# Kernel optimization log

Hardware: AMD Instinct MI355X
Metric: run time of the kernel (lower is better)

## Reference

```python
import jax, jax.numpy as jnp
import numpy as np

NUM_HEADS = 8
EPS = 1e-12  # torch F.normalize eps


def _l2norm(t):
    # F.normalize(t, dim=-1): t / max(||t||, eps)
    n = jnp.sqrt(jnp.sum(t * t, axis=-1, keepdims=True))
    return t / jnp.maximum(n, EPS)


def setup_inputs() -> dict:
    key = jax.random.key(0)
    ks = jax.random.split(key, 4)
    B, C, H, W = 16, 384, 32, 32
    x = jax.random.normal(ks[0], (B, C, H, W), dtype=jnp.float32)
    temperature = jnp.ones((NUM_HEADS, 1, 1), dtype=jnp.float32)
    qkv_w = jax.random.normal(ks[1], (3 * C, C), dtype=jnp.float32) * (1.0 / np.sqrt(C))
    qkv_b = jnp.zeros((3 * C,), dtype=jnp.float32)
    proj_w = jax.random.normal(ks[2], (C, C), dtype=jnp.float32) * (1.0 / np.sqrt(C))
    proj_b = jnp.zeros((C,), dtype=jnp.float32)
    return {"x": x, "temperature": temperature, "qkv_w": qkv_w,
            "qkv_b": qkv_b, "proj_w": proj_w, "proj_b": proj_b}


def reference(x, temperature, qkv_w, qkv_b, proj_w, proj_b):
    B, C, H, W = x.shape
    nH = NUM_HEADS
    hd = C // nH
    N = H * W
    x_flat = x.reshape(B, C, N).transpose(0, 2, 1)            # [B, N, C]
    qkv = x_flat @ qkv_w.T + qkv_b                             # [B, N, 3C]
    qkv = qkv.reshape(B, N, 3, nH, hd).transpose(2, 0, 3, 1, 4)  # [3, B, nH, N, hd]
    q, k, v = qkv[0], qkv[1], qkv[2]
    q = _l2norm(q)
    k = _l2norm(k)
    attn = jnp.einsum('bhnd,bhmd->bhnm', q, k) * temperature   # [B, nH, N, N]
    attn = jax.nn.softmax(attn, axis=-1)
    out = jnp.einsum('bhnm,bhmd->bhnd', attn, v)               # [B, nH, N, hd]
    out = out.transpose(0, 2, 1, 3).reshape(B, N, C)           # [B, N, C]
    out = out @ proj_w.T + proj_b
    return out.transpose(0, 2, 1).reshape(B, C, H, W)
```

## Files before the change

### kernel.cpp

```cpp
#include <hip/hip_runtime.h>
#include <hip/hip_bf16.h>

#define Bb   16
#define Cc   384
#define Nn   1024
#define NH   8
#define HD   48
#define C3   1152
#define D64  64

typedef _Float16 f16x8 __attribute__((ext_vector_type(8)));
typedef __fp16   h16x2 __attribute__((ext_vector_type(2)));
typedef float    f32x4 __attribute__((ext_vector_type(4)));
typedef unsigned short ushort8 __attribute__((ext_vector_type(8)));

__device__ inline unsigned short f2h(float f) {
  union { _Float16 h; unsigned short u; } cv;
  cv.h = (_Float16)f;
  return cv.u;
}
__device__ inline unsigned int pk2u(float a, float b) {
  union { h16x2 v; unsigned int u; } cv;
  cv.v = __builtin_amdgcn_cvt_pkrtz(a, b);
  return cv.u;
}
__device__ inline void plswap(unsigned int &a, unsigned int &b) {
  asm("v_permlane16_swap_b32 %0, %1" : "+v"(a), "+v"(b));
}
__device__ inline f16x8 mk8(unsigned int a, unsigned int b,
                            unsigned int c, unsigned int d) {
  union { unsigned int u[4]; f16x8 h; } cv;
  cv.u[0] = a; cv.u[1] = b; cv.u[2] = c; cv.u[3] = d;
  return cv.h;
}

__device__ inline void gload_lds16(const unsigned short* g, unsigned short* l) {
  __builtin_amdgcn_global_load_lds(
      (const __attribute__((address_space(1))) void*)g,
      (__attribute__((address_space(3))) void*)l, 16, 0, 0);
}

__global__ __launch_bounds__(256) void prep_kernel(
    const float* __restrict__ qkv_w, const float* __restrict__ pw,
    unsigned short* __restrict__ wqh, unsigned short* __restrict__ pwh,
    unsigned short* __restrict__ vt) {
  const int bid = blockIdx.x;
  if (bid < 1728) {
    int i = bid * 256 + threadIdx.x;
    wqh[i] = f2h(qkv_w[i]);
  } else if (bid < 2304) {
    int i = (bid - 1728) * 256 + threadIdx.x;
    pwh[i] = f2h(pw[i]);
  } else {
    int idx8 = (bid - 2304) * 256 + threadIdx.x;
    int bh = idx8 >> 11;
    int rem = idx8 & 2047;
    int row = 48 + (rem >> 7);
    int col = (rem & 127) * 8;
    unsigned short fill = (row == 48) ? (unsigned short)0x3C00 : (unsigned short)0;
    ushort8 v;
#pragma unroll
    for (int j = 0; j < 8; j++) v[j] = fill;
    *(ushort8*)(vt + (size_t)bh * D64 * Nn + (size_t)row * Nn + col) = v;
  }
}

__global__ __launch_bounds__(256) void xsplit_kernel(
    const float* __restrict__ x, unsigned short* __restrict__ xh) {
  __shared__ float tile[64][65];
  const int b  = blockIdx.z;
  const int c0 = blockIdx.y * 64;
  const int n0 = blockIdx.x * 64;
  const int t  = threadIdx.x;
  const int rl = t >> 2, sc = (t & 3) * 16;
  {
    const float* src = x + ((size_t)b * Cc + c0 + rl) * Nn + n0 + sc;
#pragma unroll
    for (int i = 0; i < 4; i++) {
      float4 v = *(const float4*)(src + i * 4);
      tile[rl][sc + i * 4 + 0] = v.x; tile[rl][sc + i * 4 + 1] = v.y;
      tile[rl][sc + i * 4 + 2] = v.z; tile[rl][sc + i * 4 + 3] = v.w;
    }
  }
  __syncthreads();
  {
    ushort8 h0, h1;
#pragma unroll
    for (int i = 0; i < 8; i++) h0[i] = f2h(tile[sc + i][rl]);
#pragma unroll
    for (int i = 0; i < 8; i++) h1[i] = f2h(tile[sc + 8 + i][rl]);
    size_t dst = ((size_t)b * Nn + n0 + rl) * Cc + c0 + sc;
    *(ushort8*)(xh + dst) = h0; *(ushort8*)(xh + dst + 8) = h1;
  }
}

__global__ __launch_bounds__(256, 4) void qkv_mfma(
    const unsigned short* __restrict__ wh,
    const unsigned short* __restrict__ xh,
    const float* __restrict__ bias, const float* __restrict__ temp,
    unsigned short* __restrict__ qh, unsigned short* __restrict__ kh,
    unsigned short* __restrict__ vt) {
  __shared__ unsigned short lds[128 * 136];
  unsigned short* Ash = lds;
  unsigned short* Bsh = lds + 6144;

  const int b  = blockIdx.z;
  const int yb = blockIdx.y;
  const int j0 = yb * 96;
  const int n0 = blockIdx.x * 128;
  const int tid = threadIdx.x;
  const int wave = tid >> 6, lane = tid & 63;
  const int quad = lane >> 4, l16 = lane & 15;
  const int wm = (wave >> 1) * 48, wn = (wave & 1) * 64;
  const int hs = wave >> 1;

  f32x4 acc[3][4];
#pragma unroll
  for (int mi = 0; mi < 3; mi++)
#pragma unroll
    for (int ni = 0; ni < 4; ni++) acc[mi][ni] = (f32x4){0.f, 0.f, 0.f, 0.f};

  const int sw = l16 & 7;

  for (int c0 = 0; c0 < Cc; c0 += 64) {
    __syncthreads();
#pragma unroll
    for (int s = 0; s < 3; s++) {
      int r  = s * 32 + wave * 8 + (lane >> 3);
      int cg = ((lane & 7) ^ (lane >> 3)) * 8;
      gload_lds16(wh + (size_t)(j0 + r) * Cc + c0 + cg,
                  &Ash[(s * 32 + wave * 8) * 64]);
    }
#pragma unroll
    for (int s = 0; s < 4; s++) {
      int r  = s * 32 + wave * 8 + (lane >> 3);
      int cg = ((lane & 7) ^ (lane >> 3)) * 8;
      gload_lds16(xh + ((size_t)b * Nn + n0 + r) * Cc + c0 + cg,
                  &Bsh[(s * 32 + wave * 8) * 64]);
    }
    __syncthreads();

#pragma unroll
    for (int ks = 0; ks < 64; ks += 32) {
      const int ach = (((ks >> 3) + quad) ^ sw) * 8;
      f16x8 ah[3], bh[4];
#pragma unroll
      for (int mi = 0; mi < 3; mi++)
        ah[mi] = *(const f16x8*)&Ash[(wm + mi * 16 + l16) * 64 + ach];
#pragma unroll
      for (int ni = 0; ni < 4; ni++)
        bh[ni] = *(const f16x8*)&Bsh[(wn + ni * 16 + l16) * 64 + ach];
#pragma unroll
      for (int mi = 0; mi < 3; mi++)
#pragma unroll
        for (int ni = 0; ni < 4; ni++)
          acc[mi][ni] = __builtin_amdgcn_mfma_f32_16x16x32_f16(ah[mi], bh[ni], acc[mi][ni], 0, 0, 0);
    }
  }

  const int part = yb >> 2;
  const int tq   = yb & 3;
  float bv[3][4];
#pragma unroll
  for (int mi = 0; mi < 3; mi++)
#pragma unroll
    for (int r = 0; r < 4; r++)
      bv[mi][r] = bias[j0 + wm + mi * 16 + quad * 4 + r];

  if (part < 2) {
    unsigned short* dst = part ? kh : qh;
    const float tmul = part ? 1.0f : temp[2 * tq + hs] * 1.44269504f;
    __syncthreads();
#pragma unroll
    for (int ni = 0; ni < 4; ni++) {
      float vals[3][4];
      float ss = 0.f;
#pragma unroll
      for (int mi = 0; mi < 3; mi++)
#pragma unroll
        for (int r = 0; r < 4; r++) {
          float v = acc[mi][ni][r] + bv[mi][r];
          vals[mi][r] = v; ss += v * v;
        }
      ss += __shfl_xor(ss, 16);
      ss += __shfl_xor(ss, 32);
      float scale = tmul / fmaxf(sqrtf(ss), 1e-12f);
      int n = wn + ni * 16 + l16;
#pragma unroll
      for (int mi = 0; mi < 3; mi++) {
        ushort4 sv;
        sv.x = f2h(vals[mi][0] * scale);
        sv.y = f2h(vals[mi][1] * scale);
        sv.z = f2h(vals[mi][2] * scale);
        sv.w = f2h(vals[mi][3] * scale);
        *(ushort4*)&lds[n * 136 + hs * 64 + mi * 16 + quad * 4] = sv;
      }
    }
    {
      int n = tid >> 1, h2 = tid & 1;
      ushort8 z = {0, 0, 0, 0, 0, 0, 0, 0};
      *(ushort8*)&lds[n * 136 + h2 * 64 + 48] = z;
      *(ushort8*)&lds[n * 136 + h2 * 64 + 56] = z;
    }
    __syncthreads();
#pragma unroll
    for (int it = 0; it < 8; it++) {
      int n = wave * 32 + it * 4 + (lane >> 4);
      int chunk = lane & 15;
      int hs3 = chunk >> 3, c8 = (chunk & 7) * 8;
      int h = 2 * tq + hs3;
      ushort8 v = *(const ushort8*)&lds[n * 136 + hs3 * 64 + c8];
      *(ushort8*)(dst + ((size_t)(b * NH + h) * Nn + n0 + n) * D64 + c8) = v;
    }
  } else {
    const int h = 2 * tq + hs;
#pragma unroll
    for (int mi = 0; mi < 3; mi++) {
#pragma unroll
      for (int r = 0; r < 4; r++) {
        int d = mi * 16 + quad * 4 + r;
        unsigned short* vrow = vt + ((size_t)(b * NH + h) * D64 + d) * Nn;
#pragma unroll
        for (int ni = 0; ni < 4; ni++) {
          int n = n0 + wn + ni * 16 + l16;
          vrow[n] = f2h(acc[mi][ni][r] + bv[mi][r]);
        }
      }
    }
  }
}

__global__ __launch_bounds__(256, 4) void attn_mfma(
    const unsigned short* __restrict__ qh, const unsigned short* __restrict__ kh,
    const unsigned short* __restrict__ vt,
    unsigned short* __restrict__ obh) {
  __shared__ __align__(16) unsigned short Kt[2][64 * 64];
  __shared__ __align__(16) unsigned short Vt[2][64 * 64];

  const int bid = blockIdx.x;
  const int hb = bid & 127;
  const int q0 = (bid >> 7) * 128;
  const int b = hb >> 3, h = hb & 7;
  const int tid = threadIdx.x;
  const int wave = tid >> 6, lane = tid & 63;
  const int quad = lane >> 4, l16 = lane & 15;
  const int qsw = ((quad & 1) << 1) | (quad >> 1);
  const int sx = (l16 & 7) * 8;

  const size_t headQ = ((size_t)(b * NH + h) * Nn) * D64;
  const unsigned short* Qg = qh + headQ + (size_t)(q0 + wave * 32) * D64;
  const unsigned short* Kg = kh + headQ;
  const unsigned short* Vg = vt + ((size_t)(b * NH + h) * D64) * Nn;

  f16x8 qa0[2], qa1[2];
#pragma unroll
  for (int m = 0; m < 2; m++) {
    qa0[m] = *(const f16x8*)(Qg + (m * 16 + l16) * D64 + quad * 8);
    qa1[m] = *(const f16x8*)(Qg + (m * 16 + l16) * D64 + quad * 8 + 32);
  }

  f32x4 oacc[2][4];
#pragma unroll
  for (int m = 0; m < 2; m++)
#pragma unroll
    for (int g = 0; g < 4; g++) oacc[m][g] = (f32x4){0.f, 0.f, 0.f, 0.f};
  const f32x4 zf = (f32x4){0.f, 0.f, 0.f, 0.f};

  const int srow = lane >> 3;
  const int scol = ((lane & 7) ^ srow) * 8;
  const int r0 = wave * 16;
  const unsigned short* KgS = Kg + (size_t)(r0 + srow) * D64 + scol;
  const unsigned short* VgS = Vg + (size_t)(r0 + srow) * Nn + scol;

  gload_lds16(KgS,           &Kt[0][r0 * 64]);
  gload_lds16(KgS + 8 * D64, &Kt[0][(r0 + 8) * 64]);
  gload_lds16(VgS,           &Vt[0][r0 * 64]);
  gload_lds16(VgS + 8 * Nn,  &Vt[0][(r0 + 8) * 64]);

  for (int kt = 0; kt < Nn / 64; kt++) {
    __syncthreads();
    const int cur = kt & 1;
    if (kt < Nn / 64 - 1) {
      const unsigned short* kn = KgS + (size_t)(kt + 1) * 64 * D64;
      const unsigned short* vn = VgS + (size_t)(kt + 1) * 64;
      gload_lds16(kn,           &Kt[cur ^ 1][r0 * 64]);
      gload_lds16(kn + 8 * D64, &Kt[cur ^ 1][(r0 + 8) * 64]);
      gload_lds16(vn,           &Vt[cur ^ 1][r0 * 64]);
      gload_lds16(vn + 8 * Nn,  &Vt[cur ^ 1][(r0 + 8) * 64]);
    }
    const unsigned short* Kl = Kt[cur];
    const unsigned short* Vl = Vt[cur];

    f32x4 sT[2][4];
    __builtin_amdgcn_s_setprio(1);
#pragma unroll
    for (int g = 0; g < 4; g++) {
      const unsigned short* kb = Kl + (g * 16 + l16) * 64;
      const int go = (quad * 8) ^ sx;
      f16x8 kf0 = *(const f16x8*)&kb[go];
      f16x8 kf1 = *(const f16x8*)&kb[go ^ 32];
#pragma unroll
      for (int m = 0; m < 2; m++) {
        f32x4 s = __builtin_amdgcn_mfma_f32_16x16x32_f16(kf0, qa0[m], zf, 0, 0, 0);
        sT[m][g] = __builtin_amdgcn_mfma_f32_16x16x32_f16(kf1, qa1[m], s, 0, 0, 0);
      }
    }
    __builtin_amdgcn_s_setprio(0);

    unsigned int w0[2][4], w1[2][4];
#pragma unroll
    for (int m = 0; m < 2; m++)
#pragma unroll
      for (int g = 0; g < 4; g++) {
        float e0 = __builtin_amdgcn_exp2f(sT[m][g][0]);
        float e1 = __builtin_amdgcn_exp2f(sT[m][g][1]);
        float e2 = __builtin_amdgcn_exp2f(sT[m][g][2]);
        float e3 = __builtin_amdgcn_exp2f(sT[m][g][3]);
        w0[m][g] = pk2u(e0, e1);
        w1[m][g] = pk2u(e2, e3);
      }

    f16x8 pa[2][2];
#pragma unroll
    for (int m = 0; m < 2; m++) {
      plswap(w0[m][0], w0[m][1]);
      plswap(w1[m][0], w1[m][1]);
      plswap(w0[m][2], w0[m][3]);
      plswap(w1[m][2], w1[m][3]);
      pa[m][0] = mk8(w0[m][0], w1[m][0], w0[m][1], w1[m][1]);
      pa[m][1] = mk8(w0[m][2], w1[m][2], w0[m][3], w1[m][3]);
    }

    __builtin_amdgcn_s_setprio(1);
#pragma unroll
    for (int g = 0; g < 4; g++) {
      const unsigned short* vb = Vl + (g * 16 + l16) * 64;
      const int go = (qsw * 8) ^ sx;
      f16x8 vf0 = *(const f16x8*)&vb[go];
      f16x8 vf1 = *(const f16x8*)&vb[go ^ 32];
#pragma unroll
      for (int m = 0; m < 2; m++) {
        oacc[m][g] = __builtin_amdgcn_mfma_f32_16x16x32_f16(vf0, pa[m][0], oacc[m][g], 0, 0, 0);
        oacc[m][g] = __builtin_amdgcn_mfma_f32_16x16x32_f16(vf1, pa[m][1], oacc[m][g], 0, 0, 0);
      }
    }
    __builtin_amdgcn_s_setprio(0);
  }

#pragma unroll
  for (int m = 0; m < 2; m++) {
    float inv = __builtin_amdgcn_rcpf(__shfl(oacc[m][3][0], l16));
    size_t obase = ((size_t)b * Nn + q0 + wave * 32 + m * 16 + l16) * Cc + h * HD;
#pragma unroll
    for (int g = 0; g < 3; g++) {
      ushort4 sv;
      sv.x = f2h(oacc[m][g][0] * inv);
      sv.y = f2h(oacc[m][g][1] * inv);
      sv.z = f2h(oacc[m][g][2] * inv);
      sv.w = f2h(oacc[m][g][3] * inv);
      *(ushort4*)(obh + obase + g * 16 + quad * 4) = sv;
    }
  }
}

__global__ __launch_bounds__(256, 4) void proj_mfma(
    const unsigned short* __restrict__ pwh,
    const unsigned short* __restrict__ obh,
    const float* __restrict__ pb, float* __restrict__ out) {
  __shared__ unsigned short Ash[128 * 64];
  __shared__ unsigned short Bsh[128 * 64];
  const int b  = blockIdx.z;
  const int c0m = blockIdx.y * 128;
  const int n0 = blockIdx.x * 128;
  const int tid = threadIdx.x;
  const int wave = tid >> 6, lane = tid & 63;
  const int quad = lane >> 4, l16 = lane & 15;
  const int wm = (wave >> 1) * 64, wn = (wave & 1) * 64;

  f32x4 acc[4][4];
#pragma unroll
  for (int mi = 0; mi < 4; mi++)
#pragma unroll
    for (int ni = 0; ni < 4; ni++) acc[mi][ni] = (f32x4){0.f, 0.f, 0.f, 0.f};

  const int sw = l16 & 7;

  for (int j0 = 0; j0 < Cc; j0 += 64) {
    __syncthreads();
#pragma unroll
    for (int s = 0; s < 4; s++) {
      int r  = s * 32 + wave * 8 + (lane >> 3);
      int cg = ((lane & 7) ^ (lane >> 3)) * 8;
      gload_lds16(pwh + (size_t)(c0m + r) * Cc + j0 + cg,
                  &Ash[(s * 32 + wave * 8) * 64]);
      gload_lds16(obh + ((size_t)b * Nn + n0 + r) * Cc + j0 + cg,
                  &Bsh[(s * 32 + wave * 8) * 64]);
    }
    __syncthreads();

#pragma unroll
    for (int ks = 0; ks < 64; ks += 32) {
      const int ach = (((ks >> 3) + quad) ^ sw) * 8;
      f16x8 ah[4], bh[4];
#pragma unroll
      for (int mi = 0; mi < 4; mi++)
        ah[mi] = *(const f16x8*)&Ash[(wm + mi * 16 + l16) * 64 + ach];
#pragma unroll
      for (int ni = 0; ni < 4; ni++)
        bh[ni] = *(const f16x8*)&Bsh[(wn + ni * 16 + l16) * 64 + ach];
#pragma unroll
      for (int mi = 0; mi < 4; mi++)
#pragma unroll
        for (int ni = 0; ni < 4; ni++)
          acc[mi][ni] = __builtin_amdgcn_mfma_f32_16x16x32_f16(ah[mi], bh[ni], acc[mi][ni], 0, 0, 0);
    }
  }

#pragma unroll
  for (int mi = 0; mi < 4; mi++) {
#pragma unroll
    for (int r = 0; r < 4; r++) {
      int c = c0m + wm + mi * 16 + quad * 4 + r;
      float bvv = pb[c];
#pragma unroll
      for (int ni = 0; ni < 4; ni++) {
        int n = n0 + wn + ni * 16 + l16;
        out[((size_t)b * Cc + c) * Nn + n] = acc[mi][ni][r] + bvv;
      }
    }
  }
}

extern "C" void kernel_launch(void* const* d_in, const int* in_sizes, int n_in,
                              void* d_out, int out_size, void* d_ws, size_t ws_size,
                              hipStream_t stream) {
  const float* x     = (const float*)d_in[0];
  const float* temp  = (const float*)d_in[1];
  const float* qkv_w = (const float*)d_in[2];
  const float* qkv_b = (const float*)d_in[3];
  const float* pw    = (const float*)d_in[4];
  const float* pb    = (const float*)d_in[5];
  float* out = (float*)d_out;

  const size_t QKN = (size_t)Bb * NH * Nn * D64;
  const size_t WQN = (size_t)C3 * Cc;
  const size_t PWN = (size_t)Cc * Cc;

  unsigned short* Qh  = (unsigned short*)d_ws;
  unsigned short* Kh  = Qh + QKN;
  unsigned short* VhT = Kh + QKN;
  unsigned short* Wqh = VhT + QKN;
  unsigned short* Pwh = Wqh + WQN;
  unsigned short* Xth = Pwh + PWN;
  unsigned short* Obh = Xth;

  prep_kernel<<<3328, 256, 0, stream>>>(qkv_w, pw, Wqh, Pwh, VhT);
  xsplit_kernel<<<dim3(Nn / 64, Cc / 64, Bb), 256, 0, stream>>>(x, Xth);
  qkv_mfma<<<dim3(Nn / 128, C3 / 96, Bb), 256, 0, stream>>>(Wqh, Xth, qkv_b, temp, Qh, Kh, VhT);
  attn_mfma<<<1024, 256, 0, stream>>>(Qh, Kh, VhT, Obh);
  proj_mfma<<<dim3(Nn / 128, Cc / 128, Bb), 256, 0, stream>>>(Pwh, Obh, pb, out);
}
```

Measured before the change: 158.6 us.

## Software-pipeline PV matmul one tile behind QK to overlap exp with MFMA

Restructures the attention loop so the P·V MFMAs for the previous key tile are issued right after the current tile's QK MFMAs, before the exp/pack work. This lets the exponentials of tile k overlap with matrix work of tile k-1. V gets a triple-buffered LDS ring with rotating pointers so the previous tile's V stays resident while the next one is loaded. The cost is extra LDS per block, which may reduce occupancy, plus more live registers for the carried P fragments.

```diff
diff --git a/kernel.cpp b/kernel.cpp
--- a/kernel.cpp
+++ b/kernel.cpp
@@ -235,7 +235,7 @@
     const unsigned short* __restrict__ vt,
     unsigned short* __restrict__ obh) {
   __shared__ __align__(16) unsigned short Kt[2][64 * 64];
-  __shared__ __align__(16) unsigned short Vt[2][64 * 64];
+  __shared__ __align__(16) unsigned short Vt[3][64 * 64];
 
   const int bid = blockIdx.x;
   const int hb = bid & 127;
@@ -277,19 +277,23 @@
   gload_lds16(VgS,           &Vt[0][r0 * 64]);
   gload_lds16(VgS + 8 * Nn,  &Vt[0][(r0 + 8) * 64]);
 
+  const unsigned short* vR = Vt[2];
+  const unsigned short* vC = Vt[0];
+  unsigned short*       vW = Vt[1];
+
+  f16x8 paP[2][2];
+
   for (int kt = 0; kt < Nn / 64; kt++) {
     __syncthreads();
-    const int cur = kt & 1;
     if (kt < Nn / 64 - 1) {
       const unsigned short* kn = KgS + (size_t)(kt + 1) * 64 * D64;
       const unsigned short* vn = VgS + (size_t)(kt + 1) * 64;
-      gload_lds16(kn,           &Kt[cur ^ 1][r0 * 64]);
-      gload_lds16(kn + 8 * D64, &Kt[cur ^ 1][(r0 + 8) * 64]);
-      gload_lds16(vn,           &Vt[cur ^ 1][r0 * 64]);
-      gload_lds16(vn + 8 * Nn,  &Vt[cur ^ 1][(r0 + 8) * 64]);
-    }
-    const unsigned short* Kl = Kt[cur];
-    const unsigned short* Vl = Vt[cur];
+      gload_lds16(kn,           &Kt[(kt + 1) & 1][r0 * 64]);
+      gload_lds16(kn + 8 * D64, &Kt[(kt + 1) & 1][(r0 + 8) * 64]);
+      gload_lds16(vn,           vW + r0 * 64);
+      gload_lds16(vn + 8 * Nn,  vW + (r0 + 8) * 64);
+    }
+    const unsigned short* Kl = Kt[kt & 1];
 
     f32x4 sT[2][4];
     __builtin_amdgcn_s_setprio(1);
@@ -303,6 +307,21 @@
       for (int m = 0; m < 2; m++) {
         f32x4 s = __builtin_amdgcn_mfma_f32_16x16x32_f16(kf0, qa0[m], zf, 0, 0, 0);
         sT[m][g] = __builtin_amdgcn_mfma_f32_16x16x32_f16(kf1, qa1[m], s, 0, 0, 0);
+      }
+    }
+
+    if (kt) {
+#pragma unroll
+      for (int g = 0; g < 4; g++) {
+        const unsigned short* vb = vR + (g * 16 + l16) * 64;
+        const int go = (qsw * 8) ^ sx;
+        f16x8 vf0 = *(const f16x8*)&vb[go];
+        f16x8 vf1 = *(const f16x8*)&vb[go ^ 32];
+#pragma unroll
+        for (int m = 0; m < 2; m++) {
+          oacc[m][g] = __builtin_amdgcn_mfma_f32_16x16x32_f16(vf0, paP[m][0], oacc[m][g], 0, 0, 0);
+          oacc[m][g] = __builtin_amdgcn_mfma_f32_16x16x32_f16(vf1, paP[m][1], oacc[m][g], 0, 0, 0);
+        }
       }
     }
     __builtin_amdgcn_s_setprio(0);
@@ -320,32 +339,33 @@
         w1[m][g] = pk2u(e2, e3);
       }
 
-    f16x8 pa[2][2];
 #pragma unroll
     for (int m = 0; m < 2; m++) {
       plswap(w0[m][0], w0[m][1]);
       plswap(w1[m][0], w1[m][1]);
       plswap(w0[m][2], w0[m][3]);
       plswap(w1[m][2], w1[m][3]);
-      pa[m][0] = mk8(w0[m][0], w1[m][0], w0[m][1], w1[m][1]);
-      pa[m][1] = mk8(w0[m][2], w1[m][2], w0[m][3], w1[m][3]);
-    }
-
-    __builtin_amdgcn_s_setprio(1);
-#pragma unroll
-    for (int g = 0; g < 4; g++) {
-      const unsigned short* vb = Vl + (g * 16 + l16) * 64;
-      const int go = (qsw * 8) ^ sx;
-      f16x8 vf0 = *(const f16x8*)&vb[go];
-      f16x8 vf1 = *(const f16x8*)&vb[go ^ 32];
-#pragma unroll
-      for (int m = 0; m < 2; m++) {
-        oacc[m][g] = __builtin_amdgcn_mfma_f32_16x16x32_f16(vf0, pa[m][0], oacc[m][g], 0, 0, 0);
-        oacc[m][g] = __builtin_amdgcn_mfma_f32_16x16x32_f16(vf1, pa[m][1], oacc[m][g], 0, 0, 0);
-      }
-    }
-    __builtin_amdgcn_s_setprio(0);
-  }
+      paP[m][0] = mk8(w0[m][0], w1[m][0], w0[m][1], w1[m][1]);
+      paP[m][1] = mk8(w0[m][2], w1[m][2], w0[m][3], w1[m][3]);
+    }
+
+    const unsigned short* t = vR; vR = vC; vC = vW; vW = (unsigned short*)t;
+  }
+
+  __builtin_amdgcn_s_setprio(1);
+#pragma unroll
+  for (int g = 0; g < 4; g++) {
+    const unsigned short* vb = vR + (g * 16 + l16) * 64;
+    const int go = (qsw * 8) ^ sx;
+    f16x8 vf0 = *(const f16x8*)&vb[go];
+    f16x8 vf1 = *(const f16x8*)&vb[go ^ 32];
+#pragma unroll
+    for (int m = 0; m < 2; m++) {
+      oacc[m][g] = __builtin_amdgcn_mfma_f32_16x16x32_f16(vf0, paP[m][0], oacc[m][g], 0, 0, 0);
+      oacc[m][g] = __builtin_amdgcn_mfma_f32_16x16x32_f16(vf1, paP[m][1], oacc[m][g], 0, 0, 0);
+    }
+  }
+  __builtin_amdgcn_s_setprio(0);
 
 #pragma unroll
   for (int m = 0; m < 2; m++) {
```

Measured after the change: 157.8 us. About the same (-0.5%).

## Double attention query tile per block to reuse K/V tiles across more queries

Applied to the files above, without the earlier changes.

Each attention block now handles 256 queries instead of 128: each wave holds 64 query rows (4 m-subtiles), so every K/V tile loaded into LDS and every K/V fragment read from LDS serves twice as many queries. The grid is halved to 512 blocks and launch bounds drop to 2 blocks per SM to leave room for the larger register footprint. The S computation is restructured per m-subtile so score and probability registers are reused across subtiles, which keeps pressure down. The risk is lower occupancy and fewer blocks per CU to hide latency, with 512 blocks over 256 CUs leaving little room for load balancing.

```diff
diff --git a/kernel.cpp b/kernel.cpp
--- a/kernel.cpp
+++ b/kernel.cpp
@@ -230,7 +230,7 @@
   }
 }
 
-__global__ __launch_bounds__(256, 4) void attn_mfma(
+__global__ __launch_bounds__(256, 2) void attn_mfma(
     const unsigned short* __restrict__ qh, const unsigned short* __restrict__ kh,
     const unsigned short* __restrict__ vt,
     unsigned short* __restrict__ obh) {
@@ -239,7 +239,7 @@
 
   const int bid = blockIdx.x;
   const int hb = bid & 127;
-  const int q0 = (bid >> 7) * 128;
+  const int q0 = (bid >> 7) * 256;
   const int b = hb >> 3, h = hb & 7;
   const int tid = threadIdx.x;
   const int wave = tid >> 6, lane = tid & 63;
@@ -248,20 +248,20 @@
   const int sx = (l16 & 7) * 8;
 
   const size_t headQ = ((size_t)(b * NH + h) * Nn) * D64;
-  const unsigned short* Qg = qh + headQ + (size_t)(q0 + wave * 32) * D64;
+  const unsigned short* Qg = qh + headQ + (size_t)(q0 + wave * 64) * D64;
   const unsigned short* Kg = kh + headQ;
   const unsigned short* Vg = vt + ((size_t)(b * NH + h) * D64) * Nn;
 
-  f16x8 qa0[2], qa1[2];
-#pragma unroll
-  for (int m = 0; m < 2; m++) {
+  f16x8 qa0[4], qa1[4];
+#pragma unroll
+  for (int m = 0; m < 4; m++) {
     qa0[m] = *(const f16x8*)(Qg + (m * 16 + l16) * D64 + quad * 8);
     qa1[m] = *(const f16x8*)(Qg + (m * 16 + l16) * D64 + quad * 8 + 32);
   }
 
-  f32x4 oacc[2][4];
-#pragma unroll
-  for (int m = 0; m < 2; m++)
+  f32x4 oacc[4][4];
+#pragma unroll
+  for (int m = 0; m < 4; m++)
 #pragma unroll
     for (int g = 0; g < 4; g++) oacc[m][g] = (f32x4){0.f, 0.f, 0.f, 0.f};
   const f32x4 zf = (f32x4){0.f, 0.f, 0.f, 0.f};
@@ -291,44 +291,42 @@
     const unsigned short* Kl = Kt[cur];
     const unsigned short* Vl = Vt[cur];
 
-    f32x4 sT[2][4];
-    __builtin_amdgcn_s_setprio(1);
+    f16x8 kf0[4], kf1[4];
 #pragma unroll
     for (int g = 0; g < 4; g++) {
       const unsigned short* kb = Kl + (g * 16 + l16) * 64;
       const int go = (quad * 8) ^ sx;
-      f16x8 kf0 = *(const f16x8*)&kb[go];
-      f16x8 kf1 = *(const f16x8*)&kb[go ^ 32];
-#pragma unroll
-      for (int m = 0; m < 2; m++) {
-        f32x4 s = __builtin_amdgcn_mfma_f32_16x16x32_f16(kf0, qa0[m], zf, 0, 0, 0);
-        sT[m][g] = __builtin_amdgcn_mfma_f32_16x16x32_f16(kf1, qa1[m], s, 0, 0, 0);
-      }
-    }
-    __builtin_amdgcn_s_setprio(0);
-
-    unsigned int w0[2][4], w1[2][4];
-#pragma unroll
-    for (int m = 0; m < 2; m++)
+      kf0[g] = *(const f16x8*)&kb[go];
+      kf1[g] = *(const f16x8*)&kb[go ^ 32];
+    }
+
+    f16x8 paP[4][2];
+#pragma unroll
+    for (int m = 0; m < 4; m++) {
+      f32x4 sT[4];
+      __builtin_amdgcn_s_setprio(1);
 #pragma unroll
       for (int g = 0; g < 4; g++) {
-        float e0 = __builtin_amdgcn_exp2f(sT[m][g][0]);
-        float e1 = __builtin_amdgcn_exp2f(sT[m][g][1]);
-        float e2 = __builtin_amdgcn_exp2f(sT[m][g][2]);
-        float e3 = __builtin_amdgcn_exp2f(sT[m][g][3]);
-        w0[m][g] = pk2u(e0, e1);
-        w1[m][g] = pk2u(e2, e3);
-      }
-
-    f16x8 pa[2][2];
-#pragma unroll
-    for (int m = 0; m < 2; m++) {
-      plswap(w0[m][0], w0[m][1]);
-      plswap(w1[m][0], w1[m][1]);
-      plswap(w0[m][2], w0[m][3]);
-      plswap(w1[m][2], w1[m][3]);
-      pa[m][0] = mk8(w0[m][0], w1[m][0], w0[m][1], w1[m][1]);
-      pa[m][1] = mk8(w0[m][2], w1[m][2], w0[m][3], w1[m][3]);
+        f32x4 s = __builtin_amdgcn_mfma_f32_16x16x32_f16(kf0[g], qa0[m], zf, 0, 0, 0);
+        sT[g] = __builtin_amdgcn_mfma_f32_16x16x32_f16(kf1[g], qa1[m], s, 0, 0, 0);
+      }
+      __builtin_amdgcn_s_setprio(0);
+      unsigned int w0[4], w1[4];
+#pragma unroll
+      for (int g = 0; g < 4; g++) {
+        float e0 = __builtin_amdgcn_exp2f(sT[g][0]);
+        float e1 = __builtin_amdgcn_exp2f(sT[g][1]);
+        float e2 = __builtin_amdgcn_exp2f(sT[g][2]);
+        float e3 = __builtin_amdgcn_exp2f(sT[g][3]);
+        w0[g] = pk2u(e0, e1);
+        w1[g] = pk2u(e2, e3);
+      }
+      plswap(w0[0], w0[1]);
+      plswap(w1[0], w1[1]);
+      plswap(w0[2], w0[3]);
+      plswap(w1[2], w1[3]);
+      paP[m][0] = mk8(w0[0], w1[0], w0[1], w1[1]);
+      paP[m][1] = mk8(w0[2], w1[2], w0[3], w1[3]);
     }
 
     __builtin_amdgcn_s_setprio(1);
@@ -339,18 +337,18 @@
       f16x8 vf0 = *(const f16x8*)&vb[go];
       f16x8 vf1 = *(const f16x8*)&vb[go ^ 32];
 #pragma unroll
-      for (int m = 0; m < 2; m++) {
-        oacc[m][g] = __builtin_amdgcn_mfma_f32_16x16x32_f16(vf0, pa[m][0], oacc[m][g], 0, 0, 0);
-        oacc[m][g] = __builtin_amdgcn_mfma_f32_16x16x32_f16(vf1, pa[m][1], oacc[m][g], 0, 0, 0);
+      for (int m = 0; m < 4; m++) {
+        oacc[m][g] = __builtin_amdgcn_mfma_f32_16x16x32_f16(vf0, paP[m][0], oacc[m][g], 0, 0, 0);
+        oacc[m][g] = __builtin_amdgcn_mfma_f32_16x16x32_f16(vf1, paP[m][1], oacc[m][g], 0, 0, 0);
       }
     }
     __builtin_amdgcn_s_setprio(0);
   }
 
 #pragma unroll
-  for (int m = 0; m < 2; m++) {
+  for (int m = 0; m < 4; m++) {
     float inv = __builtin_amdgcn_rcpf(__shfl(oacc[m][3][0], l16));
-    size_t obase = ((size_t)b * Nn + q0 + wave * 32 + m * 16 + l16) * Cc + h * HD;
+    size_t obase = ((size_t)b * Nn + q0 + wave * 64 + m * 16 + l16) * Cc + h * HD;
 #pragma unroll
     for (int g = 0; g < 3; g++) {
       ushort4 sv;
@@ -457,6 +455,6 @@
   prep_kernel<<<3328, 256, 0, stream>>>(qkv_w, pw, Wqh, Pwh, VhT);
   xsplit_kernel<<<dim3(Nn / 64, Cc / 64, Bb), 256, 0, stream>>>(x, Xth);
   qkv_mfma<<<dim3(Nn / 128, C3 / 96, Bb), 256, 0, stream>>>(Wqh, Xth, qkv_b, temp, Qh, Kh, VhT);
-  attn_mfma<<<1024, 256, 0, stream>>>(Qh, Kh, VhT, Obh);
+  attn_mfma<<<512, 256, 0, stream>>>(Qh, Kh, VhT, Obh);
   proj_mfma<<<dim3(Nn / 128, Cc / 128, Bb), 256, 0, stream>>>(Pwh, Obh, pb, out);
 }
```

Result: faster. 155.1 us (-2.2%).

## Load K/V fragments directly from global memory in attention kernel

Applied to the files above, without the earlier changes.

Removes the double-buffered LDS staging of K and V tiles and the per-tile barriers; each wave now reads its MFMA operand fragments straight from global memory, relying on L1/L2 caching for reuse across the four waves. This drops the sync and LDS traffic, but global load latency now sits on the critical path without an explicit prefetch, and each K/V tile is fetched by every wave. The exp/pack loop is also restructured per m to shorten register lifetimes.

```diff
diff --git a/kernel.cpp b/kernel.cpp
--- a/kernel.cpp
+++ b/kernel.cpp
@@ -234,9 +234,6 @@
     const unsigned short* __restrict__ qh, const unsigned short* __restrict__ kh,
     const unsigned short* __restrict__ vt,
     unsigned short* __restrict__ obh) {
-  __shared__ __align__(16) unsigned short Kt[2][64 * 64];
-  __shared__ __align__(16) unsigned short Vt[2][64 * 64];
-
   const int bid = blockIdx.x;
   const int hb = bid & 127;
   const int q0 = (bid >> 7) * 128;
@@ -245,7 +242,6 @@
   const int wave = tid >> 6, lane = tid & 63;
   const int quad = lane >> 4, l16 = lane & 15;
   const int qsw = ((quad & 1) << 1) | (quad >> 1);
-  const int sx = (l16 & 7) * 8;
 
   const size_t headQ = ((size_t)(b * NH + h) * Nn) * D64;
   const unsigned short* Qg = qh + headQ + (size_t)(q0 + wave * 32) * D64;
@@ -266,39 +262,20 @@
     for (int g = 0; g < 4; g++) oacc[m][g] = (f32x4){0.f, 0.f, 0.f, 0.f};
   const f32x4 zf = (f32x4){0.f, 0.f, 0.f, 0.f};
 
-  const int srow = lane >> 3;
-  const int scol = ((lane & 7) ^ srow) * 8;
-  const int r0 = wave * 16;
-  const unsigned short* KgS = Kg + (size_t)(r0 + srow) * D64 + scol;
-  const unsigned short* VgS = Vg + (size_t)(r0 + srow) * Nn + scol;
-
-  gload_lds16(KgS,           &Kt[0][r0 * 64]);
-  gload_lds16(KgS + 8 * D64, &Kt[0][(r0 + 8) * 64]);
-  gload_lds16(VgS,           &Vt[0][r0 * 64]);
-  gload_lds16(VgS + 8 * Nn,  &Vt[0][(r0 + 8) * 64]);
+  const unsigned short* Kl = Kg + (size_t)l16 * D64 + quad * 8;
+  const unsigned short* Vl = Vg + (size_t)l16 * Nn + qsw * 8;
 
   for (int kt = 0; kt < Nn / 64; kt++) {
-    __syncthreads();
-    const int cur = kt & 1;
-    if (kt < Nn / 64 - 1) {
-      const unsigned short* kn = KgS + (size_t)(kt + 1) * 64 * D64;
-      const unsigned short* vn = VgS + (size_t)(kt + 1) * 64;
-      gload_lds16(kn,           &Kt[cur ^ 1][r0 * 64]);
-      gload_lds16(kn + 8 * D64, &Kt[cur ^ 1][(r0 + 8) * 64]);
-      gload_lds16(vn,           &Vt[cur ^ 1][r0 * 64]);
-      gload_lds16(vn + 8 * Nn,  &Vt[cur ^ 1][(r0 + 8) * 64]);
-    }
-    const unsigned short* Kl = Kt[cur];
-    const unsigned short* Vl = Vt[cur];
+    const unsigned short* Kt0 = Kl + (size_t)(kt * 64) * D64;
+    const unsigned short* Vt0 = Vl + kt * 64;
 
     f32x4 sT[2][4];
     __builtin_amdgcn_s_setprio(1);
 #pragma unroll
     for (int g = 0; g < 4; g++) {
-      const unsigned short* kb = Kl + (g * 16 + l16) * 64;
-      const int go = (quad * 8) ^ sx;
-      f16x8 kf0 = *(const f16x8*)&kb[go];
-      f16x8 kf1 = *(const f16x8*)&kb[go ^ 32];
+      const unsigned short* kb = Kt0 + (size_t)(g * 16) * D64;
+      f16x8 kf0 = *(const f16x8*)kb;
+      f16x8 kf1 = *(const f16x8*)(kb + 32);
 #pragma unroll
       for (int m = 0; m < 2; m++) {
         f32x4 s = __builtin_amdgcn_mfma_f32_16x16x32_f16(kf0, qa0[m], zf, 0, 0, 0);
@@ -307,37 +284,33 @@
     }
     __builtin_amdgcn_s_setprio(0);
 
-    unsigned int w0[2][4], w1[2][4];
-#pragma unroll
-    for (int m = 0; m < 2; m++)
+    f16x8 pa[2][2];
+#pragma unroll
+    for (int m = 0; m < 2; m++) {
+      unsigned int w0[4], w1[4];
 #pragma unroll
       for (int g = 0; g < 4; g++) {
         float e0 = __builtin_amdgcn_exp2f(sT[m][g][0]);
         float e1 = __builtin_amdgcn_exp2f(sT[m][g][1]);
         float e2 = __builtin_amdgcn_exp2f(sT[m][g][2]);
         float e3 = __builtin_amdgcn_exp2f(sT[m][g][3]);
-        w0[m][g] = pk2u(e0, e1);
-        w1[m][g] = pk2u(e2, e3);
-      }
-
-    f16x8 pa[2][2];
-#pragma unroll
-    for (int m = 0; m < 2; m++) {
-      plswap(w0[m][0], w0[m][1]);
-      plswap(w1[m][0], w1[m][1]);
-      plswap(w0[m][2], w0[m][3]);
-      plswap(w1[m][2], w1[m][3]);
-      pa[m][0] = mk8(w0[m][0], w1[m][0], w0[m][1], w1[m][1]);
-      pa[m][1] = mk8(w0[m][2], w1[m][2], w0[m][3], w1[m][3]);
+        w0[g] = pk2u(e0, e1);
+        w1[g] = pk2u(e2, e3);
+      }
+      plswap(w0[0], w0[1]);
+      plswap(w1[0], w1[1]);
+      plswap(w0[2], w0[3]);
+      plswap(w1[2], w1[3]);
+      pa[m][0] = mk8(w0[0], w1[0], w0[1], w1[1]);
+      pa[m][1] = mk8(w0[2], w1[2], w0[3], w1[3]);
     }
 
     __builtin_amdgcn_s_setprio(1);
 #pragma unroll
     for (int g = 0; g < 4; g++) {
-      const unsigned short* vb = Vl + (g * 16 + l16) * 64;
-      const int go = (qsw * 8) ^ sx;
-      f16x8 vf0 = *(const f16x8*)&vb[go];
-      f16x8 vf1 = *(const f16x8*)&vb[go ^ 32];
+      const unsigned short* vb = Vt0 + (size_t)(g * 16) * Nn;
+      f16x8 vf0 = *(const f16x8*)vb;
+      f16x8 vf1 = *(const f16x8*)(vb + 32);
 #pragma unroll
       for (int m = 0; m < 2; m++) {
         oacc[m][g] = __builtin_amdgcn_mfma_f32_16x16x32_f16(vf0, pa[m][0], oacc[m][g], 0, 0, 0);
```

Result: slower. 235.5 us (+48.5%).
